# Optimization experiments

Measured on AMD Instinct MI355X. Metric: run time of the kernel, lower is better.

Reference implementation:

```python
import jax, jax.numpy as jnp
import numpy as np

B, S, D, N = 16, 1024, 512, 2048
SPECTRAL_RADIUS = 0.95
SPARSITY = 0.01  # effective_sparsity = max(0.01, 5/N) = 0.01 for N=2048


def setup_inputs() -> dict:
    key = jax.random.key(0)
    k_x, k_fb, k_wraw, k_mask, k_win, k_wfb = jax.random.split(key, 6)
    x_seq = jax.random.normal(k_x, (B, S, D), dtype=jnp.float32)
    feedback_seq = jax.random.normal(k_fb, (B, S, D), dtype=jnp.float32)
    initial_state = jnp.zeros((B, N), dtype=jnp.float32)
    # Fixed random reservoir: sparse gaussian rescaled to spectral radius ~0.95.
    # For an NxN gaussian with density p, spectral radius ~= sqrt(N*p), so we
    # rescale by SPECTRAL_RADIUS / sqrt(N*p) (the torch code uses the exact
    # max eigenvalue; this approximation preserves the same math structure).
    W_raw = jax.random.normal(k_wraw, (N, N), dtype=jnp.float32)
    mask = (jax.random.uniform(k_mask, (N, N)) < SPARSITY).astype(jnp.float32)
    W_res = W_raw * mask * (SPECTRAL_RADIUS / jnp.sqrt(N * SPARSITY))
    W_in = jax.random.normal(k_win, (N, D), dtype=jnp.float32) * 0.1
    W_fb = jax.random.normal(k_wfb, (N, D), dtype=jnp.float32) * 0.1
    return {
        "x_seq": x_seq,
        "feedback_seq": feedback_seq,
        "initial_state": initial_state,
        "W_res": W_res,
        "W_in": W_in,
        "W_fb": W_fb,
    }


def reference(x_seq, feedback_seq, initial_state, W_res, W_in, W_fb):
    # Precompute input + feedback projections as one batched GEMM each
    # (same math as per-step einsums: 'bi,ni->bn' == x @ W.T).
    drive = jnp.einsum("bsd,nd->sbn", x_seq, W_in) + jnp.einsum(
        "bsd,nd->sbn", feedback_seq, W_fb
    )  # (S, B, N)

    def step(state, drive_t):
        # pre = state @ W_res.T + W_in x_t + W_fb fb_t
        new_state = jnp.tanh(state @ W_res.T + drive_t)
        return new_state, new_state

    _, states = jax.lax.scan(step, initial_state, drive)  # (S, B, N)
    return jnp.transpose(states, (1, 0, 2))  # (B, S, N)
```

## Files before the change

### kernel.cpp

```cpp
#include <hip/hip_runtime.h>
#include <stdint.h>

typedef unsigned short u16;
typedef unsigned int   u32;
typedef __attribute__((ext_vector_type(8))) short short8;
typedef __attribute__((ext_vector_type(4))) float f32x4;

#define CAP   52

__device__ __forceinline__ u16 rne_bf16(float f){
  u32 u = __float_as_uint(f);
  u32 r = (u + 0x7fffu + ((u >> 16) & 1u)) >> 16;
  return (u16)r;
}
__device__ __forceinline__ float bf16_to_f(u16 h){
  return __uint_as_float(((u32)h) << 16);
}
__device__ __forceinline__ float tanh_fast(float x){
  float e = __expf(2.0f * x);
  return 1.0f - 2.0f / (e + 1.0f);
}

__global__ __launch_bounds__(256) void pack_a_k(const float* __restrict__ x,
                                                const float* __restrict__ fb,
                                                u16* __restrict__ A){
  int idx = blockIdx.x * 256 + threadIdx.x;
  int m = idx >> 9, d = idx & 511;
  float xv = x[idx];
  float fv = fb[idx];
  u16 xh = rne_bf16(xv); u16 xl = rne_bf16(xv - bf16_to_f(xh));
  u16 fh = rne_bf16(fv); u16 fl = rne_bf16(fv - bf16_to_f(fh));
  size_t base = (size_t)m * 2048;
  A[base + d]        = xh;
  A[base + 512 + d]  = fh;
  A[base + 1024 + d] = xl;
  A[base + 1536 + d] = fl;
}

__global__ __launch_bounds__(256) void pack_b_k(const float* __restrict__ Win,
                                                const float* __restrict__ Wfb,
                                                const int* __restrict__ rowperm,
                                                u16* __restrict__ Bm){
  int idx = blockIdx.x * 256 + threadIdx.x;
  int n = idx >> 9, d = idx & 511;
  int row = rowperm[n];
  float iv = Win[(size_t)row * 512 + d];
  float fv = Wfb[(size_t)row * 512 + d];
  u16 ih = rne_bf16(iv); u16 il = rne_bf16(iv - bf16_to_f(ih));
  u16 fh = rne_bf16(fv); u16 fl = rne_bf16(fv - bf16_to_f(fh));
  size_t base = (size_t)n * 3072;
  Bm[base + d]        = ih;
  Bm[base + 512 + d]  = fh;
  Bm[base + 1024 + d] = ih;
  Bm[base + 1536 + d] = fh;
  Bm[base + 2048 + d] = il;
  Bm[base + 2560 + d] = fl;
}

#define GLDS(gp, lp) __builtin_amdgcn_global_load_lds( \
    (const __attribute__((address_space(1))) void*)(gp), \
    (__attribute__((address_space(3))) void*)(lp), 16, 0, 0)

__global__ __launch_bounds__(256) void gemm_k(const u16* __restrict__ A,
                                              const u16* __restrict__ Bm,
                                              float* __restrict__ C){
  __shared__ __align__(16) u16 As[128 * 32];
  __shared__ __align__(16) u16 Bs[128 * 32];
  const int tid = threadIdx.x;
  const int w = tid >> 6, l = tid & 63;
  const int bid = blockIdx.x;
  const int mt = bid >> 4, nt = bid & 15;
  const int m0 = mt * 128, n0 = nt * 128;
  const int srow = tid >> 2;
  const int scol = (tid & 3) * 8;
  const int wr = w & 1, wc = w >> 1;
  const int lhi = l >> 4, llo = l & 15;

  f32x4 acc[4][4];
  #pragma unroll
  for (int i = 0; i < 4; i++)
    #pragma unroll
    for (int j = 0; j < 4; j++)
      acc[i][j] = (f32x4){0.f, 0.f, 0.f, 0.f};

  for (int kt = 0; kt < 96; ++kt){
    int k = kt * 32;
    int keff = (k >= 2048) ? (k - 2048) : k;
    #pragma unroll
    for (int r = 0; r < 2; r++){
      const u16* ga = A  + (size_t)(m0 + r * 64 + srow) * 2048 + keff + scol;
      GLDS(ga, &As[r * 2048 + w * 512]);
      const u16* gb = Bm + (size_t)(n0 + r * 64 + srow) * 3072 + k + scol;
      GLDS(gb, &Bs[r * 2048 + w * 512]);
    }
    __syncthreads();
    short8 af[4], bf[4];
    #pragma unroll
    for (int i = 0; i < 4; i++){
      af[i] = *(const short8*)&As[(wr * 64 + i * 16 + llo) * 32 + lhi * 8];
      bf[i] = *(const short8*)&Bs[(wc * 64 + i * 16 + llo) * 32 + lhi * 8];
    }
    #pragma unroll
    for (int i = 0; i < 4; i++)
      #pragma unroll
      for (int j = 0; j < 4; j++)
        acc[i][j] = __builtin_amdgcn_mfma_f32_16x16x32_bf16(af[i], bf[j], acc[i][j], 0, 0, 0);
    __syncthreads();
  }
  #pragma unroll
  for (int i = 0; i < 4; i++)
    #pragma unroll
    for (int j = 0; j < 4; j++)
      #pragma unroll
      for (int rg = 0; rg < 4; rg++){
        int mr = m0 + wr * 64 + i * 16 + lhi * 4 + rg;
        int nc = n0 + wc * 64 + j * 16 + llo;
        C[(size_t)mr * 2048 + nc] = acc[i][j][rg];
      }
}

__global__ __launch_bounds__(256) void count_k(const float* __restrict__ W,
                                               int* __restrict__ nnz){
  int gt = blockIdx.x * 256 + threadIdx.x;
  int row = gt >> 6, l = gt & 63;
  const float* wr = W + (size_t)row * 2048;
  int c = 0;
  for (int i = 0; i < 32; i++) c += (wr[i * 64 + l] != 0.0f) ? 1 : 0;
  for (int off = 32; off; off >>= 1) c += __shfl_down(c, off, 64);
  if (l == 0) nnz[row] = c;
}

__global__ __launch_bounds__(1024) void sort_k(const int* __restrict__ nnz,
                                               u32* __restrict__ rowsp,
                                               int* __restrict__ L1a,
                                               int* __restrict__ rowperm){
  __shared__ int hist[64], off[64], cur[64];
  __shared__ int order[2048];
  int tid = threadIdx.x;
  if (tid < 64){ hist[tid] = 0; cur[tid] = 0; }
  __syncthreads();
  for (int r = tid; r < 2048; r += 1024){
    int b = nnz[r]; if (b > 63) b = 63;
    atomicAdd(&hist[b], 1);
  }
  __syncthreads();
  if (tid == 0){
    int run = 0;
    for (int b = 63; b >= 0; b--){ off[b] = run; run += hist[b]; }
  }
  __syncthreads();
  for (int r = tid; r < 2048; r += 1024){
    int b = nnz[r]; if (b > 63) b = 63;
    int pos = off[b] + atomicAdd(&cur[b], 1);
    order[pos] = r;
  }
  __syncthreads();
  int rA = order[tid], rB = order[2047 - tid];
  rowsp[tid] = (u32)rA | ((u32)rB << 16);
  L1a[tid] = nnz[rA];
  rowperm[tid] = rA;
  rowperm[tid + 1024] = rB;
}

__global__ __launch_bounds__(256) void fill_k(const float* __restrict__ W,
                                              const u32* __restrict__ rowsp,
                                              u32* __restrict__ raw){
  int gt = blockIdx.x * 256 + threadIdx.x;
  int p = gt >> 6, l = gt & 63;
  u32 rp = rowsp[p];
  int rA = (int)(rp & 0xffffu), rB = (int)(rp >> 16);
  int base = 0;
  for (int h = 0; h < 2; h++){
    int row = h ? rB : rA;
    const float* wr = W + (size_t)row * 2048;
    int cnt = 0;
    for (int i = 0; i < 32; i++){
      int c = i * 64 + l;
      float v = wr[c];
      unsigned long long m = __ballot(v != 0.0f);
      int pre = __popcll(m & ((1ull << l) - 1ull));
      if (v != 0.0f){
        int s = base + cnt + pre;
        if (s < CAP){
          u32 u = __float_as_uint(v);
          u = ((u + 0x1000u) & 0xFFFFE000u) | (u32)c;
          raw[s * 1024 + p] = u;
        }
      }
      cnt += __popcll(m);
    }
    base += cnt;
  }
}

__global__ __launch_bounds__(64) void sched_k(const u32* __restrict__ raw,
                                              u32* __restrict__ wpk,
                                              const u32* __restrict__ rowsp,
                                              const int* __restrict__ nnz){
  __shared__ u32 pool[CAP * 64];
  __shared__ int cnt[64];
  const int lane = threadIdx.x;
  const int p = blockIdx.x * 64 + lane;
  const int hb = (lane >> 5) << 5;
  u32 rp = rowsp[p];
  int rA = (int)(rp & 0xffffu), rB = (int)(rp >> 16);
  int L1 = nnz[rA]; if (L1 > CAP) L1 = CAP;
  int nT = L1 + nnz[rB]; if (nT > CAP) nT = CAP;
  for (int k = 0; k < CAP; k++) pool[k * 64 + lane] = raw[k * 1024 + p];

  unsigned long long used = 0ull;
  for (int s = 0; s < CAP; s++){
    cnt[lane] = 0;
    u32 word;
    if (s < nT){
      int lo = (s < L1) ? 0 : L1;
      int hi = (s < L1) ? L1 : nT;
      int chosen = -1;
      for (int capc = 1; chosen < 0; capc++){
        for (int j = lo; j < hi; j++){
          if (used & (1ull << j)) continue;
          int bk = (int)(pool[j * 64 + lane] & 31u);
          int old = atomicAdd(&cnt[hb + bk], 1);
          if (old < capc){ chosen = j; break; }
          atomicSub(&cnt[hb + bk], 1);
        }
      }
      used |= 1ull << chosen;
      u32 r = pool[chosen * 64 + lane];
      u32 vb = r & 0xFFFFE000u;
      u32 ad = (r & 0x7FFu) << 2;
      word = ((vb - ad + 0x1000u) & 0xFFFFE000u) + ad;
    } else {
      int bsel = -1;
      for (int capc = 1; bsel < 0; capc++){
        for (int bb = 0; bb < 32; bb++){
          int bk = (bb + lane) & 31;
          int old = atomicAdd(&cnt[hb + bk], 1);
          if (old < capc){ bsel = bk; break; }
          atomicSub(&cnt[hb + bk], 1);
        }
      }
      word = (u32)bsel << 2;
    }
    wpk[s * 1024 + p] = word;
  }
}

__global__ __attribute__((amdgpu_flat_work_group_size(1024, 1024),
                          amdgpu_waves_per_eu(4, 4)))
void rnn_k(float* __restrict__ out,
           const float* __restrict__ init,
           const u32* __restrict__ wpkg,
           const u32* __restrict__ rowsp,
           const int* __restrict__ L1a){
  const int tid = threadIdx.x, b = blockIdx.x;
  u32 wk[CAP];
  #pragma unroll
  for (int k = 0; k < CAP; k++) wk[k] = wpkg[k * 1024 + tid];
  u32 rp = rowsp[tid];
  int rA = (int)(rp & 0xffffu), rB = (int)(rp >> 16);
  int L1 = L1a[tid];

  __shared__ float st[2048];
  st[tid]        = init[(size_t)b * 2048 + tid];
  st[tid + 1024] = init[(size_t)b * 2048 + tid + 1024];
  __syncthreads();
  const char* stb = (const char*)st;

  float* ob = out + (size_t)b * 1024 * 2048;
  float dA = __builtin_nontemporal_load(&ob[tid]);
  float dB = __builtin_nontemporal_load(&ob[tid + 1024]);
  for (int t = 0; t < 1024; t++){
    float* orow = ob + (size_t)t * 2048;
    const float* nrow = ob + (size_t)((t + 1) & 1023) * 2048;
    float dA2 = __builtin_nontemporal_load(&nrow[tid]);
    float dB2 = __builtin_nontemporal_load(&nrow[tid + 1024]);
    float aAll = 0.f, aA = 0.f;
    #pragma unroll
    for (int k = 0; k < CAP; k++){
      u32 w = wk[k];
      float sv = *(const float*)(stb + (w & 0x1FFCu));
      float pv = __uint_as_float(w) * sv;
      aAll += pv;
      aA += (k < L1) ? pv : 0.0f;
    }
    float preA = aA + dA;
    float preB = (aAll - aA) + dB;
    __syncthreads();
    float sA = tanh_fast(preA);
    float sB = tanh_fast(preB);
    st[rA] = sA; st[rB] = sB;
    __syncthreads();
    __builtin_nontemporal_store(st[tid], &orow[tid]);
    __builtin_nontemporal_store(st[tid + 1024], &orow[tid + 1024]);
    dA = dA2; dB = dB2;
  }
}

extern "C" void kernel_launch(void* const* d_in, const int* in_sizes, int n_in,
                              void* d_out, int out_size, void* d_ws, size_t ws_size,
                              hipStream_t stream) {
  const float* x    = (const float*)d_in[0];
  const float* fb   = (const float*)d_in[1];
  const float* init = (const float*)d_in[2];
  const float* Wres = (const float*)d_in[3];
  const float* Win  = (const float*)d_in[4];
  const float* Wfb  = (const float*)d_in[5];
  float* out = (float*)d_out;

  char* w8 = (char*)d_ws;
  u16*  A_pack = (u16*)(w8);
  u16*  B_pack = (u16*)(w8 + 67108864);
  u32*  wpk    = (u32*) (w8 + 79691776);
  int*  nnz    = (int*) (w8 + 79904768);
  u32*  rowsp  = (u32*) (w8 + 79912960);
  int*  L1a    = (int*) (w8 + 79917056);
  int*  rowperm= (int*) (w8 + 79921152);
  u32*  raw    = (u32*) out;

  pack_a_k<<<32768, 256, 0, stream>>>(x, fb, A_pack);
  count_k<<<512, 256, 0, stream>>>(Wres, nnz);
  sort_k<<<1, 1024, 0, stream>>>(nnz, rowsp, L1a, rowperm);
  pack_b_k<<<4096, 256, 0, stream>>>(Win, Wfb, rowperm, B_pack);
  fill_k<<<256, 256, 0, stream>>>(Wres, rowsp, raw);
  sched_k<<<16, 64, 0, stream>>>(raw, wpk, rowsp, nnz);
  gemm_k<<<2048, 256, 0, stream>>>(A_pack, B_pack, out);
  rnn_k<<<16, 1024, 0, stream>>>(out, init, wpk, rowsp, L1a);
}
```

Baseline: 3.085 ms.

## Double-buffer RNN state to drop a barrier and fuse schedule into GEMM

The recurrent kernel now keeps two state buffers and alternates between them, which removes one of the two __syncthreads per timestep. It encodes row membership in the low mantissa bit of each weight (stored at half value), so two FMAs (S1±S2) recover both row sums without per-k select logic. The scheduling kernel is merged into the GEMM launch as 16 extra blocks so it overlaps the GEMM, and its raw scratch moves from the output buffer to the workspace. The price is a slight precision change from the sign-bit trick and doubled LDS for the state.

```diff
diff --git a/kernel.cpp b/kernel.cpp
--- a/kernel.cpp
+++ b/kernel.cpp
@@ -57,68 +57,6 @@
   Bm[base + 2560 + d] = fl;
 }
 
-#define GLDS(gp, lp) __builtin_amdgcn_global_load_lds( \
-    (const __attribute__((address_space(1))) void*)(gp), \
-    (__attribute__((address_space(3))) void*)(lp), 16, 0, 0)
-
-__global__ __launch_bounds__(256) void gemm_k(const u16* __restrict__ A,
-                                              const u16* __restrict__ Bm,
-                                              float* __restrict__ C){
-  __shared__ __align__(16) u16 As[128 * 32];
-  __shared__ __align__(16) u16 Bs[128 * 32];
-  const int tid = threadIdx.x;
-  const int w = tid >> 6, l = tid & 63;
-  const int bid = blockIdx.x;
-  const int mt = bid >> 4, nt = bid & 15;
-  const int m0 = mt * 128, n0 = nt * 128;
-  const int srow = tid >> 2;
-  const int scol = (tid & 3) * 8;
-  const int wr = w & 1, wc = w >> 1;
-  const int lhi = l >> 4, llo = l & 15;
-
-  f32x4 acc[4][4];
-  #pragma unroll
-  for (int i = 0; i < 4; i++)
-    #pragma unroll
-    for (int j = 0; j < 4; j++)
-      acc[i][j] = (f32x4){0.f, 0.f, 0.f, 0.f};
-
-  for (int kt = 0; kt < 96; ++kt){
-    int k = kt * 32;
-    int keff = (k >= 2048) ? (k - 2048) : k;
-    #pragma unroll
-    for (int r = 0; r < 2; r++){
-      const u16* ga = A  + (size_t)(m0 + r * 64 + srow) * 2048 + keff + scol;
-      GLDS(ga, &As[r * 2048 + w * 512]);
-      const u16* gb = Bm + (size_t)(n0 + r * 64 + srow) * 3072 + k + scol;
-      GLDS(gb, &Bs[r * 2048 + w * 512]);
-    }
-    __syncthreads();
-    short8 af[4], bf[4];
-    #pragma unroll
-    for (int i = 0; i < 4; i++){
-      af[i] = *(const short8*)&As[(wr * 64 + i * 16 + llo) * 32 + lhi * 8];
-      bf[i] = *(const short8*)&Bs[(wc * 64 + i * 16 + llo) * 32 + lhi * 8];
-    }
-    #pragma unroll
-    for (int i = 0; i < 4; i++)
-      #pragma unroll
-      for (int j = 0; j < 4; j++)
-        acc[i][j] = __builtin_amdgcn_mfma_f32_16x16x32_bf16(af[i], bf[j], acc[i][j], 0, 0, 0);
-    __syncthreads();
-  }
-  #pragma unroll
-  for (int i = 0; i < 4; i++)
-    #pragma unroll
-    for (int j = 0; j < 4; j++)
-      #pragma unroll
-      for (int rg = 0; rg < 4; rg++){
-        int mr = m0 + wr * 64 + i * 16 + lhi * 4 + rg;
-        int nc = n0 + wc * 64 + j * 16 + llo;
-        C[(size_t)mr * 2048 + nc] = acc[i][j][rg];
-      }
-}
-
 __global__ __launch_bounds__(256) void count_k(const float* __restrict__ W,
                                                int* __restrict__ nnz){
   int gt = blockIdx.x * 256 + threadIdx.x;
@@ -132,7 +70,6 @@
 
 __global__ __launch_bounds__(1024) void sort_k(const int* __restrict__ nnz,
                                                u32* __restrict__ rowsp,
-                                               int* __restrict__ L1a,
                                                int* __restrict__ rowperm){
   __shared__ int hist[64], off[64], cur[64];
   __shared__ int order[2048];
@@ -157,7 +94,6 @@
   __syncthreads();
   int rA = order[tid], rB = order[2047 - tid];
   rowsp[tid] = (u32)rA | ((u32)rB << 16);
-  L1a[tid] = nnz[rA];
   rowperm[tid] = rA;
   rowperm[tid + 1024] = rB;
 }
@@ -182,8 +118,8 @@
       if (v != 0.0f){
         int s = base + cnt + pre;
         if (s < CAP){
-          u32 u = __float_as_uint(v);
-          u = ((u + 0x1000u) & 0xFFFFE000u) | (u32)c;
+          u32 u = __float_as_uint(0.5f * v);
+          u = ((u + 0x1000u) & 0xFFFFE000u) | ((u32)h << 11) | (u32)c;
           raw[s * 1024 + p] = u;
         }
       }
@@ -193,57 +129,119 @@
   }
 }
 
-__global__ __launch_bounds__(64) void sched_k(const u32* __restrict__ raw,
-                                              u32* __restrict__ wpk,
-                                              const u32* __restrict__ rowsp,
-                                              const int* __restrict__ nnz){
+#define GLDS(gp, lp) __builtin_amdgcn_global_load_lds( \
+    (const __attribute__((address_space(1))) void*)(gp), \
+    (__attribute__((address_space(3))) void*)(lp), 16, 0, 0)
+
+__global__ __launch_bounds__(256) void gemmsched_k(const u16* __restrict__ A,
+                                                   const u16* __restrict__ Bm,
+                                                   float* __restrict__ C,
+                                                   const u32* __restrict__ raw,
+                                                   u32* __restrict__ wpk,
+                                                   const u32* __restrict__ rowsp,
+                                                   const int* __restrict__ nnz){
+  __shared__ __align__(16) u16 As[128 * 32];
+  __shared__ __align__(16) u16 Bs[128 * 32];
   __shared__ u32 pool[CAP * 64];
   __shared__ int cnt[64];
-  const int lane = threadIdx.x;
-  const int p = blockIdx.x * 64 + lane;
-  const int hb = (lane >> 5) << 5;
-  u32 rp = rowsp[p];
-  int rA = (int)(rp & 0xffffu), rB = (int)(rp >> 16);
-  int L1 = nnz[rA]; if (L1 > CAP) L1 = CAP;
-  int nT = L1 + nnz[rB]; if (nT > CAP) nT = CAP;
-  for (int k = 0; k < CAP; k++) pool[k * 64 + lane] = raw[k * 1024 + p];
-
-  unsigned long long used = 0ull;
-  for (int s = 0; s < CAP; s++){
-    cnt[lane] = 0;
-    u32 word;
-    if (s < nT){
-      int lo = (s < L1) ? 0 : L1;
-      int hi = (s < L1) ? L1 : nT;
-      int chosen = -1;
-      for (int capc = 1; chosen < 0; capc++){
-        for (int j = lo; j < hi; j++){
-          if (used & (1ull << j)) continue;
-          int bk = (int)(pool[j * 64 + lane] & 31u);
-          int old = atomicAdd(&cnt[hb + bk], 1);
-          if (old < capc){ chosen = j; break; }
-          atomicSub(&cnt[hb + bk], 1);
+
+  if (blockIdx.x < 16){
+    const int lane = threadIdx.x;
+    if (lane >= 64) return;
+    const int p = blockIdx.x * 64 + lane;
+    const int hb = (lane >> 5) << 5;
+    u32 rp = rowsp[p];
+    int nT = nnz[rp & 0xffffu] + nnz[rp >> 16];
+    if (nT > CAP) nT = CAP;
+    for (int k = 0; k < CAP; k++) pool[k * 64 + lane] = raw[k * 1024 + p];
+    unsigned long long used = 0ull;
+    for (int s = 0; s < CAP; s++){
+      cnt[lane] = 0;
+      u32 word;
+      if (s < nT){
+        int chosen = -1;
+        for (int capc = 1; chosen < 0; capc++){
+          for (int j = 0; j < nT; j++){
+            if (used & (1ull << j)) continue;
+            int bk = (int)(pool[j * 64 + lane] & 31u);
+            int old = atomicAdd(&cnt[hb + bk], 1);
+            if (old < capc){ chosen = j; break; }
+            atomicSub(&cnt[hb + bk], 1);
+          }
         }
+        used |= 1ull << chosen;
+        u32 r = pool[chosen * 64 + lane];
+        u32 vb = r & 0xFFFFE000u;
+        u32 low = ((r & 0x7FFu) << 2) | ((r >> 11) & 1u);
+        word = ((vb - low + 0x1000u) & 0xFFFFE000u) + low;
+      } else {
+        int bsel = -1;
+        for (int capc = 1; bsel < 0; capc++){
+          for (int bb = 0; bb < 32; bb++){
+            int bk = (bb + lane) & 31;
+            int old = atomicAdd(&cnt[hb + bk], 1);
+            if (old < capc){ bsel = bk; break; }
+            atomicSub(&cnt[hb + bk], 1);
+          }
+        }
+        word = (u32)bsel << 2;
       }
-      used |= 1ull << chosen;
-      u32 r = pool[chosen * 64 + lane];
-      u32 vb = r & 0xFFFFE000u;
-      u32 ad = (r & 0x7FFu) << 2;
-      word = ((vb - ad + 0x1000u) & 0xFFFFE000u) + ad;
-    } else {
-      int bsel = -1;
-      for (int capc = 1; bsel < 0; capc++){
-        for (int bb = 0; bb < 32; bb++){
-          int bk = (bb + lane) & 31;
-          int old = atomicAdd(&cnt[hb + bk], 1);
-          if (old < capc){ bsel = bk; break; }
-          atomicSub(&cnt[hb + bk], 1);
-        }
+      wpk[s * 1024 + p] = word;
+    }
+    return;
+  }
+
+  const int tid = threadIdx.x;
+  const int w = tid >> 6, l = tid & 63;
+  const int bid = blockIdx.x - 16;
+  const int mt = bid >> 4, nt = bid & 15;
+  const int m0 = mt * 128, n0 = nt * 128;
+  const int srow = tid >> 2;
+  const int scol = (tid & 3) * 8;
+  const int wr = w & 1, wc = w >> 1;
+  const int lhi = l >> 4, llo = l & 15;
+
+  f32x4 acc[4][4];
+  #pragma unroll
+  for (int i = 0; i < 4; i++)
+    #pragma unroll
+    for (int j = 0; j < 4; j++)
+      acc[i][j] = (f32x4){0.f, 0.f, 0.f, 0.f};
+
+  for (int kt = 0; kt < 96; ++kt){
+    int k = kt * 32;
+    int keff = (k >= 2048) ? (k - 2048) : k;
+    #pragma unroll
+    for (int r = 0; r < 2; r++){
+      const u16* ga = A  + (size_t)(m0 + r * 64 + srow) * 2048 + keff + scol;
+      GLDS(ga, &As[r * 2048 + w * 512]);
+      const u16* gb = Bm + (size_t)(n0 + r * 64 + srow) * 3072 + k + scol;
+      GLDS(gb, &Bs[r * 2048 + w * 512]);
+    }
+    __syncthreads();
+    short8 af[4], bf[4];
+    #pragma unroll
+    for (int i = 0; i < 4; i++){
+      af[i] = *(const short8*)&As[(wr * 64 + i * 16 + llo) * 32 + lhi * 8];
+      bf[i] = *(const short8*)&Bs[(wc * 64 + i * 16 + llo) * 32 + lhi * 8];
+    }
+    #pragma unroll
+    for (int i = 0; i < 4; i++)
+      #pragma unroll
+      for (int j = 0; j < 4; j++)
+        acc[i][j] = __builtin_amdgcn_mfma_f32_16x16x32_bf16(af[i], bf[j], acc[i][j], 0, 0, 0);
+    __syncthreads();
+  }
+  #pragma unroll
+  for (int i = 0; i < 4; i++)
+    #pragma unroll
+    for (int j = 0; j < 4; j++)
+      #pragma unroll
+      for (int rg = 0; rg < 4; rg++){
+        int mr = m0 + wr * 64 + i * 16 + lhi * 4 + rg;
+        int nc = n0 + wc * 64 + j * 16 + llo;
+        C[(size_t)mr * 2048 + nc] = acc[i][j][rg];
       }
-      word = (u32)bsel << 2;
-    }
-    wpk[s * 1024 + p] = word;
-  }
 }
 
 __global__ __attribute__((amdgpu_flat_work_group_size(1024, 1024),
@@ -251,50 +249,57 @@
 void rnn_k(float* __restrict__ out,
            const float* __restrict__ init,
            const u32* __restrict__ wpkg,
-           const u32* __restrict__ rowsp,
-           const int* __restrict__ L1a){
+           const u32* __restrict__ rowsp){
   const int tid = threadIdx.x, b = blockIdx.x;
   u32 wk[CAP];
   #pragma unroll
   for (int k = 0; k < CAP; k++) wk[k] = wpkg[k * 1024 + tid];
   u32 rp = rowsp[tid];
-  int rA = (int)(rp & 0xffffu), rB = (int)(rp >> 16);
-  int L1 = L1a[tid];
-
-  __shared__ float st[2048];
+  const int rA4 = (int)(rp & 0xffffu) << 2;
+  const int rB4 = (int)(rp >> 16) << 2;
+
+  __shared__ float st[4096];
   st[tid]        = init[(size_t)b * 2048 + tid];
   st[tid + 1024] = init[(size_t)b * 2048 + tid + 1024];
   __syncthreads();
   const char* stb = (const char*)st;
+  char* stw = (char*)st;
+  const int t4a = tid << 2, t4b = (tid + 1024) << 2;
 
   float* ob = out + (size_t)b * 1024 * 2048;
   float dA = __builtin_nontemporal_load(&ob[tid]);
   float dB = __builtin_nontemporal_load(&ob[tid + 1024]);
-  for (int t = 0; t < 1024; t++){
-    float* orow = ob + (size_t)t * 2048;
-    const float* nrow = ob + (size_t)((t + 1) & 1023) * 2048;
-    float dA2 = __builtin_nontemporal_load(&nrow[tid]);
-    float dB2 = __builtin_nontemporal_load(&nrow[tid + 1024]);
-    float aAll = 0.f, aA = 0.f;
-    #pragma unroll
-    for (int k = 0; k < CAP; k++){
-      u32 w = wk[k];
-      float sv = *(const float*)(stb + (w & 0x1FFCu));
-      float pv = __uint_as_float(w) * sv;
-      aAll += pv;
-      aA += (k < L1) ? pv : 0.0f;
-    }
-    float preA = aA + dA;
-    float preB = (aAll - aA) + dB;
-    __syncthreads();
-    float sA = tanh_fast(preA);
-    float sB = tanh_fast(preB);
-    st[rA] = sA; st[rB] = sB;
-    __syncthreads();
-    __builtin_nontemporal_store(st[tid], &orow[tid]);
-    __builtin_nontemporal_store(st[tid + 1024], &orow[tid + 1024]);
-    dA = dA2; dB = dB2;
-  }
+
+#define ESN_STEP(T, RD, WR) { \
+    float* orow = ob + (size_t)(T) * 2048; \
+    const float* nrow = ob + (size_t)(((T) + 1) & 1023) * 2048; \
+    float dA2 = __builtin_nontemporal_load(&nrow[tid]); \
+    float dB2 = __builtin_nontemporal_load(&nrow[tid + 1024]); \
+    float S1 = 0.f, S2 = 0.f; \
+    _Pragma("unroll") \
+    for (int k = 0; k < CAP; k++){ \
+      u32 w = wk[k]; \
+      float sv = *(const float*)(stb + (RD) + (w & 0x1FFCu)); \
+      float wv  = __uint_as_float(w); \
+      float wv2 = __uint_as_float(w ^ (w << 31)); \
+      S1 = __builtin_fmaf(wv,  sv, S1); \
+      S2 = __builtin_fmaf(wv2, sv, S2); \
+    } \
+    float sA = tanh_fast((S1 + S2) + dA); \
+    float sB = tanh_fast((S1 - S2) + dB); \
+    *(float*)(stw + (WR) + rA4) = sA; \
+    *(float*)(stw + (WR) + rB4) = sB; \
+    __syncthreads(); \
+    __builtin_nontemporal_store(*(const float*)(stb + (WR) + t4a), &orow[tid]); \
+    __builtin_nontemporal_store(*(const float*)(stb + (WR) + t4b), &orow[tid + 1024]); \
+    dA = dA2; dB = dB2; \
+  }
+
+  for (int t = 0; t < 1024; t += 2){
+    ESN_STEP(t, 0, 8192)
+    ESN_STEP(t + 1, 8192, 0)
+  }
+#undef ESN_STEP
 }
 
 extern "C" void kernel_launch(void* const* d_in, const int* in_sizes, int n_in,
@@ -314,16 +319,14 @@
   u32*  wpk    = (u32*) (w8 + 79691776);
   int*  nnz    = (int*) (w8 + 79904768);
   u32*  rowsp  = (u32*) (w8 + 79912960);
-  int*  L1a    = (int*) (w8 + 79917056);
-  int*  rowperm= (int*) (w8 + 79921152);
-  u32*  raw    = (u32*) out;
+  int*  rowperm= (int*) (w8 + 79917056);
+  u32*  raw    = (u32*) (w8 + 79925248);
 
   pack_a_k<<<32768, 256, 0, stream>>>(x, fb, A_pack);
   count_k<<<512, 256, 0, stream>>>(Wres, nnz);
-  sort_k<<<1, 1024, 0, stream>>>(nnz, rowsp, L1a, rowperm);
+  sort_k<<<1, 1024, 0, stream>>>(nnz, rowsp, rowperm);
   pack_b_k<<<4096, 256, 0, stream>>>(Win, Wfb, rowperm, B_pack);
   fill_k<<<256, 256, 0, stream>>>(Wres, rowsp, raw);
-  sched_k<<<16, 64, 0, stream>>>(raw, wpk, rowsp, nnz);
-  gemm_k<<<2048, 256, 0, stream>>>(A_pack, B_pack, out);
-  rnn_k<<<16, 1024, 0, stream>>>(out, init, wpk, rowsp, L1a);
-}
+  gemmsched_k<<<2064, 256, 0, stream>>>(A_pack, B_pack, out, raw, wpk, rowsp, nnz);
+  rnn_k<<<16, 1024, 0, stream>>>(out, init, wpk, rowsp);
+}
```

Result: slower. 5.206 ms (+68.7%).
